# Kernel optimization log

Hardware: AMD Instinct MI355X
Metric: run time of the kernel (lower is better)

The kernel has to match this reference:

```python
import jax, jax.numpy as jnp
import numpy as np

N_MIX = 2


def setup_inputs() -> dict:
    key = jax.random.key(0)
    k1, k2, k3, k4 = jax.random.split(key, 4)
    B, d_k, N = 8, 512, 2048
    qt = jax.random.normal(k1, (B, d_k, N), dtype=jnp.float32)
    kt = jax.random.normal(k2, (B, d_k, N), dtype=jnp.float32)
    vt = jax.random.normal(k3, (B, d_k, N), dtype=jnp.float32)
    std = N_MIX ** -0.5
    weight = jax.random.uniform(k4, (N_MIX, d_k), dtype=jnp.float32, minval=-std, maxval=std)
    return {"qt": qt, "kt": kt, "vt": vt, "weight": weight}


def reference(qt, kt, vt, weight):
    # qt: [B, d_k, N], kt: [B, d_k, N2], vt: [B, d_v, N2], weight: [m, d_k]
    B, d_k, N = qt.shape
    N2 = kt.shape[2]
    m = N_MIX
    d = d_k // m
    temperature = jnp.float32(d_k ** 0.5)  # note: sqrt(d_k), not sqrt(d)

    # mixture weights pi: softmax over the m mixture components
    bar_qt = jnp.mean(qt, axis=2)  # [B, d_k]
    pi = jax.nn.softmax(jnp.einsum('md,bd->bm', weight, bar_qt), axis=1)  # [B, m]
    pi = pi.reshape(B * m, 1, 1)

    q = jnp.transpose(qt.reshape(B * m, d, N), (0, 2, 1))  # [B*m, N, d]
    k = kt.reshape(B * m, d, N2)                            # [B*m, d, N2]
    v = jnp.transpose(vt, (0, 2, 1))                        # [B, N2, d_v]

    attn = jnp.matmul(q, k) / temperature                   # [B*m, N, N2]
    attn = jax.nn.softmax(attn, axis=2)
    # dropout is identity at inference
    attn = (attn * pi).reshape(B, m, N, N2).sum(axis=1)     # [B, N, N2]

    output = jnp.matmul(attn, v)                            # [B, N, d_v]
    return output, attn
```

## Files before the change

kernel.cpp:

```cpp
#include <hip/hip_runtime.h>
#include <stdint.h>

typedef unsigned short u16;
typedef float f32x4 __attribute__((ext_vector_type(4)));
typedef _Float16 half8 __attribute__((ext_vector_type(8)));
typedef __fp16 fp16x2 __attribute__((ext_vector_type(2)));

#define B_  8
#define M_  2
#define DK_ 512
#define D_  256
#define N_  2048
#define DV_ 512

#define OUT_FLOATS (B_*N_*DV_)
#define QB_U16     (B_*M_*N_*D_)

__device__ __forceinline__ uint32_t pk16(float a, float b){
    fp16x2 h = __builtin_amdgcn_cvt_pkrtz(a, b);
    return __builtin_bit_cast(uint32_t, h);
}
__device__ __forceinline__ float h2f_lo(uint32_t u){
    return (float)__builtin_bit_cast(_Float16, (unsigned short)(u & 0xffffu));
}
__device__ __forceinline__ float h2f_hi(uint32_t u){
    return (float)__builtin_bit_cast(_Float16, (unsigned short)(u >> 16));
}

__global__ __launch_bounds__(256) void k0_transpose(const float* __restrict__ qt,
                                                    const float* __restrict__ kt,
                                                    u16* __restrict__ dstBase){
    const int it = blockIdx.x, yc = blockIdx.y, z = blockIdx.z;
    const int b = z & 7, src = z >> 3;
    const float* sp = src ? kt : qt;
    u16* dp = dstBase + (size_t)src * QB_U16;
    const int m = yc >> 2;
    const int cbase = (yc & 3) * 64;
    const int i0 = it * 64;
    __shared__ u16 lds[64 * 72];
    const int t = threadIdx.x;
    {
        const int c_loc = t >> 2;
        const int iq = (t & 3) * 16;
        const float* g = sp + (size_t)(b*DK_ + m*D_ + cbase + c_loc) * N_ + i0 + iq;
        float vv[16];
        *(float4*)&vv[0]  = *(const float4*)(g + 0);
        *(float4*)&vv[4]  = *(const float4*)(g + 4);
        *(float4*)&vv[8]  = *(const float4*)(g + 8);
        *(float4*)&vv[12] = *(const float4*)(g + 12);
        #pragma unroll
        for (int e = 0; e < 16; ++e){
            _Float16 hf = (_Float16)vv[e];
            lds[(iq + e)*72 + c_loc] = __builtin_bit_cast(unsigned short, hf);
        }
    }
    __syncthreads();
    {
        const int i_loc = t >> 2;
        const int cq = (t & 3) * 16;
        uint4 a  = *(const uint4*)&lds[i_loc*72 + cq];
        uint4 b2 = *(const uint4*)&lds[i_loc*72 + cq + 8];
        u16* o = dp + (size_t)((b*M_ + m)*N_ + i0 + i_loc) * D_ + cbase + cq;
        *(uint4*)o = a;
        *(uint4*)(o + 8) = b2;
    }
}

__global__ __launch_bounds__(256) void k0_vconv(const float* __restrict__ vt,
                                                u16* __restrict__ vB){
    size_t idx = ((size_t)blockIdx.x * 256 + threadIdx.x) * 8;
    const size_t total = (size_t)B_ * DV_ * N_;
    if (idx < total){
        float4 f0 = *(const float4*)(vt + idx);
        float4 f1 = *(const float4*)(vt + idx + 4);
        uint4 o;
        o.x = pk16(f0.x, f0.y);
        o.y = pk16(f0.z, f0.w);
        o.z = pk16(f1.x, f1.y);
        o.w = pk16(f1.z, f1.w);
        *(uint4*)(vB + idx) = o;
    }
}

__global__ __launch_bounds__(256) void k1_bar(const float* __restrict__ qt,
                                              float* __restrict__ bar){
    const int cg = blockIdx.x, b = blockIdx.y;
    const int t = threadIdx.x;
    const int c = cg*8 + (t >> 5);
    const int seg = t & 31;
    const float* g = qt + (size_t)(b*DK_ + c)*N_ + seg*64;
    float s = 0.f;
    #pragma unroll
    for (int k = 0; k < 16; ++k){
        float4 f = *(const float4*)(g + k*4);
        s += f.x + f.y + f.z + f.w;
    }
    s += __shfl_xor(s, 1); s += __shfl_xor(s, 2); s += __shfl_xor(s, 4);
    s += __shfl_xor(s, 8); s += __shfl_xor(s, 16);
    if (seg == 0) bar[b*DK_ + c] = s * (1.f / (float)N_);
}

__global__ void k2_logits(const float* __restrict__ wgt,
                          const float* __restrict__ bar,
                          float* __restrict__ wsLog){
    const int bm = blockIdx.x;
    const int b = bm >> 1, m = bm & 1;
    const int l = threadIdx.x;
    float s = 0.f;
    #pragma unroll
    for (int k = 0; k < 8; ++k){
        const int c = l + k*64;
        s += wgt[m*DK_ + c] * bar[b*DK_ + c];
    }
    s += __shfl_xor(s, 1); s += __shfl_xor(s, 2); s += __shfl_xor(s, 4);
    s += __shfl_xor(s, 8); s += __shfl_xor(s, 16); s += __shfl_xor(s, 32);
    if (l == 0) wsLog[bm] = s;
}

__global__ __launch_bounds__(256, 2) void k3_qk(const u16* __restrict__ qB,
                                                const u16* __restrict__ kB,
                                                uint32_t* __restrict__ attnE){
    const int jt = blockIdx.x, it = blockIdx.y, b = blockIdx.z;
    const int t = threadIdx.x;
    const int w = t >> 6, l = t & 63;
    const int wi = w & 1, wj = w >> 1;
    const int l15 = l & 15, lq = l >> 4;
    __shared__ u16 lds[4 * 128 * 64];

    f32x4 acc[2][4][4] = {};

    const int srow = t >> 1, shalf = t & 1;
    for (int bk = 0; bk < 4; ++bk){
        #pragma unroll
        for (int tile = 0; tile < 4; ++tile){
            const int qk = tile >> 1, m = tile & 1;
            const u16* sp = qk ? kB : qB;
            const int row0 = (qk ? jt : it) * 128;
            const u16* g = sp + (size_t)((b*M_ + m)*N_ + row0 + srow) * D_ + bk*64 + shalf*32;
            const uint4* gp = (const uint4*)g;
            uint4 v0 = gp[0], v1 = gp[1], v2 = gp[2], v3 = gp[3];
            u16* base = &lds[(tile*128 + srow) * 64];
            const int rs = srow & 7;
            *(uint4*)&base[((shalf*4 + 0) ^ rs) * 8] = v0;
            *(uint4*)&base[((shalf*4 + 1) ^ rs) * 8] = v1;
            *(uint4*)&base[((shalf*4 + 2) ^ rs) * 8] = v2;
            *(uint4*)&base[((shalf*4 + 3) ^ rs) * 8] = v3;
        }
        __syncthreads();
        #pragma unroll
        for (int ks = 0; ks < 2; ++ks){
            #pragma unroll
            for (int m = 0; m < 2; ++m){
                half8 a[4], bb[4];
                #pragma unroll
                for (int ti = 0; ti < 4; ++ti){
                    const int row = wi*64 + ti*16 + l15;
                    const int gr = (ks*4 + lq) ^ (row & 7);
                    a[ti] = *(const half8*)&lds[(m*128 + row)*64 + gr*8];
                }
                #pragma unroll
                for (int tj = 0; tj < 4; ++tj){
                    const int row = wj*64 + tj*16 + l15;
                    const int gr = (ks*4 + lq) ^ (row & 7);
                    bb[tj] = *(const half8*)&lds[((2 + m)*128 + row)*64 + gr*8];
                }
                #pragma unroll
                for (int ti = 0; ti < 4; ++ti)
                    #pragma unroll
                    for (int tj = 0; tj < 4; ++tj)
                        acc[m][ti][tj] = __builtin_amdgcn_mfma_f32_16x16x32_f16(
                            a[ti], bb[tj], acc[m][ti][tj], 0, 0, 0);
            }
        }
        __syncthreads();
    }

    const float INVT = 0.04419417382415922f;
    uint32_t* op = attnE + (size_t)b * N_ * N_;
    const int ibase = it*128 + wi*64;
    const int jbase = jt*128 + wj*64;
    #pragma unroll
    for (int ti = 0; ti < 4; ++ti){
        #pragma unroll
        for (int tj = 0; tj < 4; ++tj){
            #pragma unroll
            for (int rr = 0; rr < 4; ++rr){
                const int i = ibase + ti*16 + lq*4 + rr;
                const int j = jbase + tj*16 + l15;
                const float e0 = __expf(acc[0][ti][tj][rr] * INVT);
                const float e1 = __expf(acc[1][ti][tj][rr] * INVT);
                op[(size_t)i * N_ + j] = pk16(e0, e1);
            }
        }
    }
}

__global__ __launch_bounds__(256, 2) void k4_pv(const float* __restrict__ vt,
                                                const u16* __restrict__ vB,
                                                const float* __restrict__ wsLog,
                                                uint32_t* __restrict__ attnE,
                                                float* __restrict__ outO){
    const int itile = blockIdx.x, b = blockIdx.y;
    const int i0 = itile * 64;
    const int t = threadIdx.x, w = t >> 6, l = t & 63;
    const int l15 = l & 15, lq = l >> 4;
    __shared__ u16 v_lds[DV_ * 32];
    __shared__ float p0s[64], p1s[64];

    const float lg0 = wsLog[b*2 + 0], lg1 = wsLog[b*2 + 1];
    const float pi0 = 1.f / (1.f + __expf(lg1 - lg0));
    const float pi1 = 1.f / (1.f + __expf(lg0 - lg1));

    {
        const int rl = t >> 2, seg = t & 3;
        const uint4* e = (const uint4*)(attnE + (size_t)(b*N_ + i0 + rl)*N_ + seg*512);
        float s0 = 0.f, s1 = 0.f;
        for (int k = 0; k < 128; ++k){
            uint4 u = e[k];
            s0 += h2f_lo(u.x) + h2f_lo(u.y) + h2f_lo(u.z) + h2f_lo(u.w);
            s1 += h2f_hi(u.x) + h2f_hi(u.y) + h2f_hi(u.z) + h2f_hi(u.w);
        }
        s0 += __shfl_xor(s0, 1); s0 += __shfl_xor(s0, 2);
        s1 += __shfl_xor(s1, 1); s1 += __shfl_xor(s1, 2);
        if (seg == 0){ p0s[rl] = pi0 / s0; p1s[rl] = pi1 / s1; }
    }
    __syncthreads();

    f32x4 acc[32] = {};
    const int rl = w*16 + l15;
    const float p0 = p0s[rl], p1 = p1s[rl];
    uint32_t* erow = attnE + (size_t)(b*N_ + i0 + rl)*N_;

    for (int c = 0; c < 64; ++c){
        const int j0 = c * 32;
        {
            const int dv = t * 2;
            if (vB){
                const u16* g = vB + (size_t)(b*DV_ + dv)*N_ + j0;
                #pragma unroll
                for (int r = 0; r < 2; ++r){
                    const int dvr = dv + r;
                    const uint4* gp = (const uint4*)(g + (size_t)r * N_);
                    #pragma unroll
                    for (int q8 = 0; q8 < 4; ++q8)
                        *(uint4*)&v_lds[dvr*32 + ((q8 ^ (dvr & 3)) * 8)] = gp[q8];
                }
            } else {
                #pragma unroll
                for (int r = 0; r < 2; ++r){
                    const int dvr = dv + r;
                    const float* gr = vt + (size_t)(b*DV_ + dvr)*N_ + j0;
                    #pragma unroll
                    for (int q8 = 0; q8 < 4; ++q8){
                        float4 fA = *(const float4*)(gr + q8*8);
                        float4 fB = *(const float4*)(gr + q8*8 + 4);
                        uint4 u;
                        u.x = pk16(fA.x, fA.y);
                        u.y = pk16(fA.z, fA.w);
                        u.z = pk16(fB.x, fB.y);
                        u.w = pk16(fB.z, fB.w);
                        *(uint4*)&v_lds[dvr*32 + ((q8 ^ (dvr & 3)) * 8)] = u;
                    }
                }
            }
        }
        uint32_t* ep = erow + j0 + lq*8;
        uint4 u0 = *(const uint4*)ep;
        uint4 u1 = *(const uint4*)(ep + 4);
        float av[8];
        av[0] = p0*h2f_lo(u0.x) + p1*h2f_hi(u0.x);
        av[1] = p0*h2f_lo(u0.y) + p1*h2f_hi(u0.y);
        av[2] = p0*h2f_lo(u0.z) + p1*h2f_hi(u0.z);
        av[3] = p0*h2f_lo(u0.w) + p1*h2f_hi(u0.w);
        av[4] = p0*h2f_lo(u1.x) + p1*h2f_hi(u1.x);
        av[5] = p0*h2f_lo(u1.y) + p1*h2f_hi(u1.y);
        av[6] = p0*h2f_lo(u1.z) + p1*h2f_hi(u1.z);
        av[7] = p0*h2f_lo(u1.w) + p1*h2f_hi(u1.w);
        uint4 ua;
        ua.x = pk16(av[0], av[1]);
        ua.y = pk16(av[2], av[3]);
        ua.z = pk16(av[4], av[5]);
        ua.w = pk16(av[6], av[7]);
        union { uint4 u; half8 h; } cvt;
        cvt.u = ua;
        half8 af = cvt.h;

        __syncthreads();

        float4 w0 = make_float4(av[0], av[1], av[2], av[3]);
        float4 w1 = make_float4(av[4], av[5], av[6], av[7]);
        *(float4*)ep = w0;
        *(float4*)(ep + 4) = w1;

        #pragma unroll
        for (int n = 0; n < 32; ++n){
            const int dv = n*16 + l15;
            half8 bv = *(const half8*)&v_lds[dv*32 + ((lq ^ (dv & 3)) * 8)];
            acc[n] = __builtin_amdgcn_mfma_f32_16x16x32_f16(af, bv, acc[n], 0, 0, 0);
        }
        __syncthreads();
    }

    #pragma unroll
    for (int n = 0; n < 32; ++n){
        #pragma unroll
        for (int rr = 0; rr < 4; ++rr){
            const int i = i0 + w*16 + lq*4 + rr;
            const int dv = n*16 + l15;
            outO[(size_t)(b*N_ + i)*DV_ + dv] = acc[n][rr];
        }
    }
}

extern "C" void kernel_launch(void* const* d_in, const int* in_sizes, int n_in,
                              void* d_out, int out_size, void* d_ws, size_t ws_size,
                              hipStream_t stream){
    const float* qt  = (const float*)d_in[0];
    const float* kt  = (const float*)d_in[1];
    const float* vt  = (const float*)d_in[2];
    const float* wgt = (const float*)d_in[3];

    float* ws    = (float*)d_ws;
    float* wsLog = ws;
    float* wsBar = ws + 16;

    u16* stage = (u16*)d_out;
    u16* kB = stage + QB_U16;
    uint32_t* attnE = (uint32_t*)d_out + OUT_FLOATS;
    float* outO = (float*)d_out;

    const size_t vbBytes = (size_t)B_ * DV_ * N_ * 2;
    u16* vB = (ws_size >= (size_t)65536 + vbBytes)
                  ? (u16*)((char*)d_ws + 65536) : (u16*)nullptr;

    k0_transpose<<<dim3(32, 8, 16), 256, 0, stream>>>(qt, kt, stage);
    if (vB) k0_vconv<<<dim3(4096), 256, 0, stream>>>(vt, vB);
    k1_bar<<<dim3(64, 8), 256, 0, stream>>>(qt, wsBar);
    k2_logits<<<dim3(16), 64, 0, stream>>>(wgt, wsBar, wsLog);
    k3_qk<<<dim3(16, 16, 8), 256, 0, stream>>>(stage, kB, attnE);
    k4_pv<<<dim3(32, 8), 256, 0, stream>>>(vt, vB, wsLog, attnE, outO);
}
```

Baseline: 270.2 us.

## Split row-sum into separate kernel and double-buffer V tiles in PV kernel

Moves the per-row softmax denominator computation out of the PV kernel into a dedicated, fully parallel rowsum kernel that writes per-row scale factors to workspace. The PV kernel now runs 512 threads per block, with each half of the waves covering half the value dimension. It double-buffers V tiles in LDS, prefetching global loads two chunks ahead, and prefetches the next attention fragments. This removes the serial row-sum prologue and one barrier per iteration, at the cost of an extra launch, a second full read of the attention matrix, and doubled LDS use.

```diff
diff --git a/kernel.cpp b/kernel.cpp
--- a/kernel.cpp
+++ b/kernel.cpp
@@ -195,87 +195,124 @@
     }
 }
 
-__global__ __launch_bounds__(256, 2) void k4_pv(const float* __restrict__ vt,
-                                                const u16* __restrict__ vB,
-                                                const float* __restrict__ wsLog,
-                                                uint32_t* __restrict__ attnE,
-                                                float* __restrict__ outO){
+__global__ __launch_bounds__(256) void k35_rowsum(const uint32_t* __restrict__ attnE,
+                                                  const float* __restrict__ wsLog,
+                                                  float* __restrict__ wsScale){
+    const int blk = blockIdx.x;
+    const int b = blk >> 9;
+    const int w = threadIdx.x >> 6, l = threadIdx.x & 63;
+    const int i = (blk & 511)*4 + w;
+    const uint4* e = (const uint4*)(attnE + ((size_t)b*N_ + i)*N_);
+    float s0 = 0.f, s1 = 0.f;
+    #pragma unroll
+    for (int k = 0; k < 8; ++k){
+        uint4 u = e[k*64 + l];
+        s0 += h2f_lo(u.x) + h2f_lo(u.y) + h2f_lo(u.z) + h2f_lo(u.w);
+        s1 += h2f_hi(u.x) + h2f_hi(u.y) + h2f_hi(u.z) + h2f_hi(u.w);
+    }
+    s0 += __shfl_xor(s0, 1);  s1 += __shfl_xor(s1, 1);
+    s0 += __shfl_xor(s0, 2);  s1 += __shfl_xor(s1, 2);
+    s0 += __shfl_xor(s0, 4);  s1 += __shfl_xor(s1, 4);
+    s0 += __shfl_xor(s0, 8);  s1 += __shfl_xor(s1, 8);
+    s0 += __shfl_xor(s0, 16); s1 += __shfl_xor(s1, 16);
+    s0 += __shfl_xor(s0, 32); s1 += __shfl_xor(s1, 32);
+    if (l == 0){
+        const float lg0 = wsLog[b*2 + 0], lg1 = wsLog[b*2 + 1];
+        const float pi0 = 1.f / (1.f + __expf(lg1 - lg0));
+        const float pi1 = 1.f / (1.f + __expf(lg0 - lg1));
+        wsScale[((size_t)b*N_ + i)*2 + 0] = pi0 / s0;
+        wsScale[((size_t)b*N_ + i)*2 + 1] = pi1 / s1;
+    }
+}
+
+template<bool HASVB>
+__global__ __launch_bounds__(512) void k4_pv(const float* __restrict__ vt,
+                                             const u16* __restrict__ vB,
+                                             const float* __restrict__ wsScale,
+                                             uint32_t* __restrict__ attnE,
+                                             float* __restrict__ outO){
     const int itile = blockIdx.x, b = blockIdx.y;
     const int i0 = itile * 64;
-    const int t = threadIdx.x, w = t >> 6, l = t & 63;
+    const int t = threadIdx.x;
+    const int l = t & 63, w = t >> 6;
     const int l15 = l & 15, lq = l >> 4;
-    __shared__ u16 v_lds[DV_ * 32];
-    __shared__ float p0s[64], p1s[64];
-
-    const float lg0 = wsLog[b*2 + 0], lg1 = wsLog[b*2 + 1];
-    const float pi0 = 1.f / (1.f + __expf(lg1 - lg0));
-    const float pi1 = 1.f / (1.f + __expf(lg0 - lg1));
-
-    {
-        const int rl = t >> 2, seg = t & 3;
-        const uint4* e = (const uint4*)(attnE + (size_t)(b*N_ + i0 + rl)*N_ + seg*512);
-        float s0 = 0.f, s1 = 0.f;
-        for (int k = 0; k < 128; ++k){
-            uint4 u = e[k];
-            s0 += h2f_lo(u.x) + h2f_lo(u.y) + h2f_lo(u.z) + h2f_lo(u.w);
-            s1 += h2f_hi(u.x) + h2f_hi(u.y) + h2f_hi(u.z) + h2f_hi(u.w);
-        }
-        s0 += __shfl_xor(s0, 1); s0 += __shfl_xor(s0, 2);
-        s1 += __shfl_xor(s1, 1); s1 += __shfl_xor(s1, 2);
-        if (seg == 0){ p0s[rl] = pi0 / s0; p1s[rl] = pi1 / s1; }
-    }
+    const int rowgrp = w & 3, dvh = w >> 2;
+    __shared__ u16 v_lds[2][512 * 32];
+
+    const int rl = rowgrp*16 + l15;
+    const float2 p01 = *(const float2*)&wsScale[((size_t)(b*N_ + i0 + rl))*2];
+    const float p0 = p01.x, p1 = p01.y;
+    uint32_t* erow = attnE + (size_t)(b*N_ + i0 + rl) * N_;
+
+    const int vswz  = (t >> 2) & 3;
+    const int rslot = lq ^ (l15 >> 2);
+
+    const u16*   gv16 = vB + (size_t)(b*DV_ + t)*N_;
+    const float* gv32 = vt + (size_t)(b*DV_ + t)*N_;
+
+    uint4  rv[4];
+    float4 rf[8];
+
+    auto issue_load = [&](int c){
+        const int j0 = c*32;
+        if (HASVB){
+            const uint4* gp = (const uint4*)(gv16 + j0);
+            rv[0] = gp[0]; rv[1] = gp[1]; rv[2] = gp[2]; rv[3] = gp[3];
+        } else {
+            const float4* gp = (const float4*)(gv32 + j0);
+            #pragma unroll
+            for (int q = 0; q < 8; ++q) rf[q] = gp[q];
+        }
+    };
+    auto write_lds = [&](int buf){
+        u16* base = &v_lds[buf][t*32];
+        #pragma unroll
+        for (int G = 0; G < 4; ++G){
+            uint4 u;
+            if (HASVB){
+                u = rv[G];
+            } else {
+                u.x = pk16(rf[2*G].x,   rf[2*G].y);
+                u.y = pk16(rf[2*G].z,   rf[2*G].w);
+                u.z = pk16(rf[2*G+1].x, rf[2*G+1].y);
+                u.w = pk16(rf[2*G+1].z, rf[2*G+1].w);
+            }
+            *(uint4*)&base[(G ^ vswz)*8] = u;
+        }
+    };
+
+    f32x4 acc[16] = {};
+
+    issue_load(0);
+    write_lds(0);
+    issue_load(1);
+    uint4 e0 = *(const uint4*)(erow + lq*8);
+    uint4 e1 = *(const uint4*)(erow + lq*8 + 4);
     __syncthreads();
 
-    f32x4 acc[32] = {};
-    const int rl = w*16 + l15;
-    const float p0 = p0s[rl], p1 = p1s[rl];
-    uint32_t* erow = attnE + (size_t)(b*N_ + i0 + rl)*N_;
-
+    int cur = 0;
     for (int c = 0; c < 64; ++c){
-        const int j0 = c * 32;
-        {
-            const int dv = t * 2;
-            if (vB){
-                const u16* g = vB + (size_t)(b*DV_ + dv)*N_ + j0;
-                #pragma unroll
-                for (int r = 0; r < 2; ++r){
-                    const int dvr = dv + r;
-                    const uint4* gp = (const uint4*)(g + (size_t)r * N_);
-                    #pragma unroll
-                    for (int q8 = 0; q8 < 4; ++q8)
-                        *(uint4*)&v_lds[dvr*32 + ((q8 ^ (dvr & 3)) * 8)] = gp[q8];
-                }
-            } else {
-                #pragma unroll
-                for (int r = 0; r < 2; ++r){
-                    const int dvr = dv + r;
-                    const float* gr = vt + (size_t)(b*DV_ + dvr)*N_ + j0;
-                    #pragma unroll
-                    for (int q8 = 0; q8 < 4; ++q8){
-                        float4 fA = *(const float4*)(gr + q8*8);
-                        float4 fB = *(const float4*)(gr + q8*8 + 4);
-                        uint4 u;
-                        u.x = pk16(fA.x, fA.y);
-                        u.y = pk16(fA.z, fA.w);
-                        u.z = pk16(fB.x, fB.y);
-                        u.w = pk16(fB.z, fB.w);
-                        *(uint4*)&v_lds[dvr*32 + ((q8 ^ (dvr & 3)) * 8)] = u;
-                    }
-                }
-            }
-        }
-        uint32_t* ep = erow + j0 + lq*8;
-        uint4 u0 = *(const uint4*)ep;
-        uint4 u1 = *(const uint4*)(ep + 4);
+        if (c + 1 < 64) write_lds(cur ^ 1);
+        if (c + 2 < 64) issue_load(c + 2);
+        uint4 en0, en1;
+        if (c + 1 < 64){
+            en0 = *(const uint4*)(erow + (c+1)*32 + lq*8);
+            en1 = *(const uint4*)(erow + (c+1)*32 + lq*8 + 4);
+        }
         float av[8];
-        av[0] = p0*h2f_lo(u0.x) + p1*h2f_hi(u0.x);
-        av[1] = p0*h2f_lo(u0.y) + p1*h2f_hi(u0.y);
-        av[2] = p0*h2f_lo(u0.z) + p1*h2f_hi(u0.z);
-        av[3] = p0*h2f_lo(u0.w) + p1*h2f_hi(u0.w);
-        av[4] = p0*h2f_lo(u1.x) + p1*h2f_hi(u1.x);
-        av[5] = p0*h2f_lo(u1.y) + p1*h2f_hi(u1.y);
-        av[6] = p0*h2f_lo(u1.z) + p1*h2f_hi(u1.z);
-        av[7] = p0*h2f_lo(u1.w) + p1*h2f_hi(u1.w);
+        av[0] = p0*h2f_lo(e0.x) + p1*h2f_hi(e0.x);
+        av[1] = p0*h2f_lo(e0.y) + p1*h2f_hi(e0.y);
+        av[2] = p0*h2f_lo(e0.z) + p1*h2f_hi(e0.z);
+        av[3] = p0*h2f_lo(e0.w) + p1*h2f_hi(e0.w);
+        av[4] = p0*h2f_lo(e1.x) + p1*h2f_hi(e1.x);
+        av[5] = p0*h2f_lo(e1.y) + p1*h2f_hi(e1.y);
+        av[6] = p0*h2f_lo(e1.z) + p1*h2f_hi(e1.z);
+        av[7] = p0*h2f_lo(e1.w) + p1*h2f_hi(e1.w);
+        if (dvh == 0){
+            float* ap = (float*)(erow + c*32 + lq*8);
+            *(float4*)ap       = make_float4(av[0], av[1], av[2], av[3]);
+            *(float4*)(ap + 4) = make_float4(av[4], av[5], av[6], av[7]);
+        }
         uint4 ua;
         ua.x = pk16(av[0], av[1]);
         ua.y = pk16(av[2], av[3]);
@@ -285,28 +322,23 @@
         cvt.u = ua;
         half8 af = cvt.h;
 
+        const u16* vb = &v_lds[cur][(dvh*256 + l15)*32 + rslot*8];
+        #pragma unroll
+        for (int n = 0; n < 16; ++n){
+            half8 bv = *(const half8*)(vb + n*512);
+            acc[n] = __builtin_amdgcn_mfma_f32_16x16x32_f16(af, bv, acc[n], 0, 0, 0);
+        }
+        if (c + 1 < 64){ e0 = en0; e1 = en1; }
         __syncthreads();
-
-        float4 w0 = make_float4(av[0], av[1], av[2], av[3]);
-        float4 w1 = make_float4(av[4], av[5], av[6], av[7]);
-        *(float4*)ep = w0;
-        *(float4*)(ep + 4) = w1;
-
-        #pragma unroll
-        for (int n = 0; n < 32; ++n){
-            const int dv = n*16 + l15;
-            half8 bv = *(const half8*)&v_lds[dv*32 + ((lq ^ (dv & 3)) * 8)];
-            acc[n] = __builtin_amdgcn_mfma_f32_16x16x32_f16(af, bv, acc[n], 0, 0, 0);
-        }
-        __syncthreads();
-    }
-
-    #pragma unroll
-    for (int n = 0; n < 32; ++n){
+        cur ^= 1;
+    }
+
+    #pragma unroll
+    for (int n = 0; n < 16; ++n){
         #pragma unroll
         for (int rr = 0; rr < 4; ++rr){
-            const int i = i0 + w*16 + lq*4 + rr;
-            const int dv = n*16 + l15;
+            const int i  = i0 + rowgrp*16 + lq*4 + rr;
+            const int dv = dvh*256 + n*16 + l15;
             outO[(size_t)(b*N_ + i)*DV_ + dv] = acc[n][rr];
         }
     }
@@ -320,9 +352,10 @@
     const float* vt  = (const float*)d_in[2];
     const float* wgt = (const float*)d_in[3];
 
-    float* ws    = (float*)d_ws;
-    float* wsLog = ws;
-    float* wsBar = ws + 16;
+    float* ws      = (float*)d_ws;
+    float* wsLog   = ws;
+    float* wsBar   = ws + 16;
+    float* wsScale = (float*)((char*)d_ws + 32768);
 
     u16* stage = (u16*)d_out;
     u16* kB = stage + QB_U16;
@@ -330,13 +363,15 @@
     float* outO = (float*)d_out;
 
     const size_t vbBytes = (size_t)B_ * DV_ * N_ * 2;
-    u16* vB = (ws_size >= (size_t)65536 + vbBytes)
-                  ? (u16*)((char*)d_ws + 65536) : (u16*)nullptr;
+    u16* vB = (ws_size >= (size_t)262144 + vbBytes)
+                  ? (u16*)((char*)d_ws + 262144) : (u16*)nullptr;
 
     k0_transpose<<<dim3(32, 8, 16), 256, 0, stream>>>(qt, kt, stage);
     if (vB) k0_vconv<<<dim3(4096), 256, 0, stream>>>(vt, vB);
     k1_bar<<<dim3(64, 8), 256, 0, stream>>>(qt, wsBar);
     k2_logits<<<dim3(16), 64, 0, stream>>>(wgt, wsBar, wsLog);
     k3_qk<<<dim3(16, 16, 8), 256, 0, stream>>>(stage, kB, attnE);
-    k4_pv<<<dim3(32, 8), 256, 0, stream>>>(vt, vB, wsLog, attnE, outO);
-}
+    k35_rowsum<<<dim3(4096), 256, 0, stream>>>(attnE, wsLog, wsScale);
+    if (vB) k4_pv<true ><<<dim3(32, 8), 512, 0, stream>>>(vt, vB, wsScale, attnE, outO);
+    else    k4_pv<false><<<dim3(32, 8), 512, 0, stream>>>(vt, vB, wsScale, attnE, outO);
+}
```

Measured after the change: 238.4 us. 1.13x faster.

## Fuse row-sum and mean into producers; register-pipeline PV kernel without LDS

Applied to the files above, without the earlier changes.

The query column mean moves into the transpose kernel via atomics, dropping the separate mean kernel. Softmax row sums are now accumulated with atomics in the QK epilogue, so the PV kernel no longer re-reads each attention row just to normalise it. The PV kernel is restructured into 32-row tiles with the value dimension split across waves, loading V fragments straight from global into registers with double buffering instead of staging through LDS. In exchange it adds a workspace memset, atomic contention and more register pressure, and each wave reloads V from global memory.

```diff
diff --git a/kernel.cpp b/kernel.cpp
--- a/kernel.cpp
+++ b/kernel.cpp
@@ -29,7 +29,8 @@
 
 __global__ __launch_bounds__(256) void k0_transpose(const float* __restrict__ qt,
                                                     const float* __restrict__ kt,
-                                                    u16* __restrict__ dstBase){
+                                                    u16* __restrict__ dstBase,
+                                                    float* __restrict__ wsBar){
     const int it = blockIdx.x, yc = blockIdx.y, z = blockIdx.z;
     const int b = z & 7, src = z >> 3;
     const float* sp = src ? kt : qt;
@@ -53,6 +54,15 @@
             _Float16 hf = (_Float16)vv[e];
             lds[(iq + e)*72 + c_loc] = __builtin_bit_cast(unsigned short, hf);
         }
+        if (src == 0){
+            float s = 0.f;
+            #pragma unroll
+            for (int e = 0; e < 16; ++e) s += vv[e];
+            s += __shfl_xor(s, 1);
+            s += __shfl_xor(s, 2);
+            if ((t & 3) == 0)
+                atomicAdd(&wsBar[b*DK_ + m*D_ + cbase + c_loc], s);
+        }
     }
     __syncthreads();
     {
@@ -82,24 +92,6 @@
     }
 }
 
-__global__ __launch_bounds__(256) void k1_bar(const float* __restrict__ qt,
-                                              float* __restrict__ bar){
-    const int cg = blockIdx.x, b = blockIdx.y;
-    const int t = threadIdx.x;
-    const int c = cg*8 + (t >> 5);
-    const int seg = t & 31;
-    const float* g = qt + (size_t)(b*DK_ + c)*N_ + seg*64;
-    float s = 0.f;
-    #pragma unroll
-    for (int k = 0; k < 16; ++k){
-        float4 f = *(const float4*)(g + k*4);
-        s += f.x + f.y + f.z + f.w;
-    }
-    s += __shfl_xor(s, 1); s += __shfl_xor(s, 2); s += __shfl_xor(s, 4);
-    s += __shfl_xor(s, 8); s += __shfl_xor(s, 16);
-    if (seg == 0) bar[b*DK_ + c] = s * (1.f / (float)N_);
-}
-
 __global__ void k2_logits(const float* __restrict__ wgt,
                           const float* __restrict__ bar,
                           float* __restrict__ wsLog){
@@ -114,12 +106,13 @@
     }
     s += __shfl_xor(s, 1); s += __shfl_xor(s, 2); s += __shfl_xor(s, 4);
     s += __shfl_xor(s, 8); s += __shfl_xor(s, 16); s += __shfl_xor(s, 32);
-    if (l == 0) wsLog[bm] = s;
+    if (l == 0) wsLog[bm] = s * (1.f / (float)N_);
 }
 
 __global__ __launch_bounds__(256, 2) void k3_qk(const u16* __restrict__ qB,
                                                 const u16* __restrict__ kB,
-                                                uint32_t* __restrict__ attnE){
+                                                uint32_t* __restrict__ attnE,
+                                                float* __restrict__ wsSum){
     const int jt = blockIdx.x, it = blockIdx.y, b = blockIdx.z;
     const int t = threadIdx.x;
     const int w = t >> 6, l = t & 63;
@@ -181,6 +174,7 @@
     const int jbase = jt*128 + wj*64;
     #pragma unroll
     for (int ti = 0; ti < 4; ++ti){
+        float rs[2][4] = {};
         #pragma unroll
         for (int tj = 0; tj < 4; ++tj){
             #pragma unroll
@@ -190,124 +184,144 @@
                 const float e0 = __expf(acc[0][ti][tj][rr] * INVT);
                 const float e1 = __expf(acc[1][ti][tj][rr] * INVT);
                 op[(size_t)i * N_ + j] = pk16(e0, e1);
-            }
-        }
-    }
-}
-
+                rs[0][rr] += e0;
+                rs[1][rr] += e1;
+            }
+        }
+        #pragma unroll
+        for (int m2 = 0; m2 < 2; ++m2){
+            #pragma unroll
+            for (int rr = 0; rr < 4; ++rr){
+                float s = rs[m2][rr];
+                s += __shfl_xor(s, 1); s += __shfl_xor(s, 2);
+                s += __shfl_xor(s, 4); s += __shfl_xor(s, 8);
+                if (l15 == 0)
+                    atomicAdd(&wsSum[(size_t)(b*M_ + m2)*N_ + ibase + ti*16 + lq*4 + rr], s);
+            }
+        }
+    }
+}
+
+template<bool HASVB>
 __global__ __launch_bounds__(256, 2) void k4_pv(const float* __restrict__ vt,
                                                 const u16* __restrict__ vB,
                                                 const float* __restrict__ wsLog,
+                                                const float* __restrict__ wsSum,
                                                 uint32_t* __restrict__ attnE,
                                                 float* __restrict__ outO){
-    const int itile = blockIdx.x, b = blockIdx.y;
-    const int i0 = itile * 64;
-    const int t = threadIdx.x, w = t >> 6, l = t & 63;
+    const int tile = blockIdx.x, b = blockIdx.y;
+    const int i0 = tile * 32;
+    const int t = threadIdx.x, l = t & 63;
+    const int dvq = t >> 6;
     const int l15 = l & 15, lq = l >> 4;
-    __shared__ u16 v_lds[DV_ * 32];
-    __shared__ float p0s[64], p1s[64];
 
     const float lg0 = wsLog[b*2 + 0], lg1 = wsLog[b*2 + 1];
     const float pi0 = 1.f / (1.f + __expf(lg1 - lg0));
     const float pi1 = 1.f / (1.f + __expf(lg0 - lg1));
 
-    {
-        const int rl = t >> 2, seg = t & 3;
-        const uint4* e = (const uint4*)(attnE + (size_t)(b*N_ + i0 + rl)*N_ + seg*512);
-        float s0 = 0.f, s1 = 0.f;
-        for (int k = 0; k < 128; ++k){
-            uint4 u = e[k];
-            s0 += h2f_lo(u.x) + h2f_lo(u.y) + h2f_lo(u.z) + h2f_lo(u.w);
-            s1 += h2f_hi(u.x) + h2f_hi(u.y) + h2f_hi(u.z) + h2f_hi(u.w);
-        }
-        s0 += __shfl_xor(s0, 1); s0 += __shfl_xor(s0, 2);
-        s1 += __shfl_xor(s1, 1); s1 += __shfl_xor(s1, 2);
-        if (seg == 0){ p0s[rl] = pi0 / s0; p1s[rl] = pi1 / s1; }
-    }
-    __syncthreads();
-
-    f32x4 acc[32] = {};
-    const int rl = w*16 + l15;
-    const float p0 = p0s[rl], p1 = p1s[rl];
-    uint32_t* erow = attnE + (size_t)(b*N_ + i0 + rl)*N_;
-
-    for (int c = 0; c < 64; ++c){
-        const int j0 = c * 32;
-        {
-            const int dv = t * 2;
-            if (vB){
-                const u16* g = vB + (size_t)(b*DV_ + dv)*N_ + j0;
-                #pragma unroll
-                for (int r = 0; r < 2; ++r){
-                    const int dvr = dv + r;
-                    const uint4* gp = (const uint4*)(g + (size_t)r * N_);
-                    #pragma unroll
-                    for (int q8 = 0; q8 < 4; ++q8)
-                        *(uint4*)&v_lds[dvr*32 + ((q8 ^ (dvr & 3)) * 8)] = gp[q8];
-                }
+    float p0[2], p1[2];
+    uint32_t* erow[2];
+    #pragma unroll
+    for (int rg = 0; rg < 2; ++rg){
+        const int row = i0 + rg*16 + l15;
+        p0[rg] = pi0 / wsSum[(size_t)(b*M_ + 0)*N_ + row];
+        p1[rg] = pi1 / wsSum[(size_t)(b*M_ + 1)*N_ + row];
+        erow[rg] = attnE + (size_t)(b*N_ + row) * N_;
+    }
+
+    const u16*   vb16 = vB + (size_t)(b*DV_ + dvq*128 + l15)*N_ + lq*8;
+    const float* vb32 = vt + (size_t)(b*DV_ + dvq*128 + l15)*N_ + lq*8;
+
+    f32x4 acc[2][8] = {};
+    uint4 eA[2][2], eB[2][2];
+    half8 bA[8], bB[8];
+
+    auto loadE = [&](uint4 (&e)[2][2], int c){
+        #pragma unroll
+        for (int rg = 0; rg < 2; ++rg){
+            const uint4* p = (const uint4*)(erow[rg] + c*32 + lq*8);
+            e[rg][0] = p[0];
+            e[rg][1] = p[1];
+        }
+    };
+    auto loadB = [&](half8 (&bb)[8], int c){
+        #pragma unroll
+        for (int n = 0; n < 8; ++n){
+            if (HASVB){
+                bb[n] = *(const half8*)(vb16 + (size_t)n*16*N_ + c*32);
             } else {
-                #pragma unroll
-                for (int r = 0; r < 2; ++r){
-                    const int dvr = dv + r;
-                    const float* gr = vt + (size_t)(b*DV_ + dvr)*N_ + j0;
-                    #pragma unroll
-                    for (int q8 = 0; q8 < 4; ++q8){
-                        float4 fA = *(const float4*)(gr + q8*8);
-                        float4 fB = *(const float4*)(gr + q8*8 + 4);
-                        uint4 u;
-                        u.x = pk16(fA.x, fA.y);
-                        u.y = pk16(fA.z, fA.w);
-                        u.z = pk16(fB.x, fB.y);
-                        u.w = pk16(fB.z, fB.w);
-                        *(uint4*)&v_lds[dvr*32 + ((q8 ^ (dvr & 3)) * 8)] = u;
-                    }
-                }
-            }
-        }
-        uint32_t* ep = erow + j0 + lq*8;
-        uint4 u0 = *(const uint4*)ep;
-        uint4 u1 = *(const uint4*)(ep + 4);
-        float av[8];
-        av[0] = p0*h2f_lo(u0.x) + p1*h2f_hi(u0.x);
-        av[1] = p0*h2f_lo(u0.y) + p1*h2f_hi(u0.y);
-        av[2] = p0*h2f_lo(u0.z) + p1*h2f_hi(u0.z);
-        av[3] = p0*h2f_lo(u0.w) + p1*h2f_hi(u0.w);
-        av[4] = p0*h2f_lo(u1.x) + p1*h2f_hi(u1.x);
-        av[5] = p0*h2f_lo(u1.y) + p1*h2f_hi(u1.y);
-        av[6] = p0*h2f_lo(u1.z) + p1*h2f_hi(u1.z);
-        av[7] = p0*h2f_lo(u1.w) + p1*h2f_hi(u1.w);
-        uint4 ua;
-        ua.x = pk16(av[0], av[1]);
-        ua.y = pk16(av[2], av[3]);
-        ua.z = pk16(av[4], av[5]);
-        ua.w = pk16(av[6], av[7]);
-        union { uint4 u; half8 h; } cvt;
-        cvt.u = ua;
-        half8 af = cvt.h;
-
-        __syncthreads();
-
-        float4 w0 = make_float4(av[0], av[1], av[2], av[3]);
-        float4 w1 = make_float4(av[4], av[5], av[6], av[7]);
-        *(float4*)ep = w0;
-        *(float4*)(ep + 4) = w1;
-
-        #pragma unroll
-        for (int n = 0; n < 32; ++n){
-            const int dv = n*16 + l15;
-            half8 bv = *(const half8*)&v_lds[dv*32 + ((lq ^ (dv & 3)) * 8)];
-            acc[n] = __builtin_amdgcn_mfma_f32_16x16x32_f16(af, bv, acc[n], 0, 0, 0);
-        }
-        __syncthreads();
+                const float* p = vb32 + (size_t)n*16*N_ + c*32;
+                float4 f0 = *(const float4*)p;
+                float4 f1 = *(const float4*)(p + 4);
+                uint4 u;
+                u.x = pk16(f0.x, f0.y); u.y = pk16(f0.z, f0.w);
+                u.z = pk16(f1.x, f1.y); u.w = pk16(f1.z, f1.w);
+                union { uint4 u; half8 h; } cv; cv.u = u;
+                bb[n] = cv.h;
+            }
+        }
+    };
+
+    loadE(eA, 0);
+    loadB(bA, 0);
+
+    auto body = [&](int c, uint4 (&ec)[2][2], uint4 (&en)[2][2],
+                    half8 (&bc)[8], half8 (&bn)[8]){
+        float av[2][8];
+        half8 af[2];
+        #pragma unroll
+        for (int rg = 0; rg < 2; ++rg){
+            uint4 u0 = ec[rg][0], u1 = ec[rg][1];
+            av[rg][0] = p0[rg]*h2f_lo(u0.x) + p1[rg]*h2f_hi(u0.x);
+            av[rg][1] = p0[rg]*h2f_lo(u0.y) + p1[rg]*h2f_hi(u0.y);
+            av[rg][2] = p0[rg]*h2f_lo(u0.z) + p1[rg]*h2f_hi(u0.z);
+            av[rg][3] = p0[rg]*h2f_lo(u0.w) + p1[rg]*h2f_hi(u0.w);
+            av[rg][4] = p0[rg]*h2f_lo(u1.x) + p1[rg]*h2f_hi(u1.x);
+            av[rg][5] = p0[rg]*h2f_lo(u1.y) + p1[rg]*h2f_hi(u1.y);
+            av[rg][6] = p0[rg]*h2f_lo(u1.z) + p1[rg]*h2f_hi(u1.z);
+            av[rg][7] = p0[rg]*h2f_lo(u1.w) + p1[rg]*h2f_hi(u1.w);
+            uint4 ua;
+            ua.x = pk16(av[rg][0], av[rg][1]);
+            ua.y = pk16(av[rg][2], av[rg][3]);
+            ua.z = pk16(av[rg][4], av[rg][5]);
+            ua.w = pk16(av[rg][6], av[rg][7]);
+            union { uint4 u; half8 h; } cv; cv.u = ua;
+            af[rg] = cv.h;
+        }
+        __builtin_amdgcn_sched_barrier(0);
+        __builtin_amdgcn_s_barrier();
+        __builtin_amdgcn_sched_barrier(0);
+        if (dvq < 2){
+            float* ap = (float*)(erow[dvq] + c*32 + lq*8);
+            *(float4*)ap       = make_float4(av[dvq][0], av[dvq][1], av[dvq][2], av[dvq][3]);
+            *(float4*)(ap + 4) = make_float4(av[dvq][4], av[dvq][5], av[dvq][6], av[dvq][7]);
+        }
+        if (c < 63){
+            loadE(en, c + 1);
+            loadB(bn, c + 1);
+        }
+        #pragma unroll
+        for (int n = 0; n < 8; ++n){
+            acc[0][n] = __builtin_amdgcn_mfma_f32_16x16x32_f16(af[0], bc[n], acc[0][n], 0, 0, 0);
+            acc[1][n] = __builtin_amdgcn_mfma_f32_16x16x32_f16(af[1], bc[n], acc[1][n], 0, 0, 0);
+        }
+    };
+
+    for (int c = 0; c < 64; c += 2){
+        body(c,     eA, eB, bA, bB);
+        body(c + 1, eB, eA, bB, bA);
     }
 
     #pragma unroll
-    for (int n = 0; n < 32; ++n){
-        #pragma unroll
-        for (int rr = 0; rr < 4; ++rr){
-            const int i = i0 + w*16 + lq*4 + rr;
-            const int dv = n*16 + l15;
-            outO[(size_t)(b*N_ + i)*DV_ + dv] = acc[n][rr];
+    for (int n = 0; n < 8; ++n){
+        #pragma unroll
+        for (int rg = 0; rg < 2; ++rg){
+            #pragma unroll
+            for (int rr = 0; rr < 4; ++rr){
+                const int i  = i0 + rg*16 + lq*4 + rr;
+                const int dv = dvq*128 + n*16 + l15;
+                outO[(size_t)(b*N_ + i)*DV_ + dv] = acc[rg][n][rr];
+            }
         }
     }
 }
@@ -322,7 +336,8 @@
 
     float* ws    = (float*)d_ws;
     float* wsLog = ws;
-    float* wsBar = ws + 16;
+    float* wsBar = (float*)((char*)d_ws + 4096);
+    float* wsSum = (float*)((char*)d_ws + 65536);
 
     u16* stage = (u16*)d_out;
     u16* kB = stage + QB_U16;
@@ -330,13 +345,15 @@
     float* outO = (float*)d_out;
 
     const size_t vbBytes = (size_t)B_ * DV_ * N_ * 2;
-    u16* vB = (ws_size >= (size_t)65536 + vbBytes)
-                  ? (u16*)((char*)d_ws + 65536) : (u16*)nullptr;
-
-    k0_transpose<<<dim3(32, 8, 16), 256, 0, stream>>>(qt, kt, stage);
+    u16* vB = (ws_size >= (size_t)1048576 + vbBytes)
+                  ? (u16*)((char*)d_ws + 1048576) : (u16*)nullptr;
+
+    hipMemsetAsync(d_ws, 0, 262144, stream);
+
+    k0_transpose<<<dim3(32, 8, 16), 256, 0, stream>>>(qt, kt, stage, wsBar);
     if (vB) k0_vconv<<<dim3(4096), 256, 0, stream>>>(vt, vB);
-    k1_bar<<<dim3(64, 8), 256, 0, stream>>>(qt, wsBar);
     k2_logits<<<dim3(16), 64, 0, stream>>>(wgt, wsBar, wsLog);
-    k3_qk<<<dim3(16, 16, 8), 256, 0, stream>>>(stage, kB, attnE);
-    k4_pv<<<dim3(32, 8), 256, 0, stream>>>(vt, vB, wsLog, attnE, outO);
-}
+    k3_qk<<<dim3(16, 16, 8), 256, 0, stream>>>(stage, kB, attnE, wsSum);
+    if (vB) k4_pv<true ><<<dim3(64, 8), 256, 0, stream>>>(vt, vB, wsLog, wsSum, attnE, outO);
+    else    k4_pv<false><<<dim3(64, 8), 256, 0, stream>>>(vt, vB, wsLog, wsSum, attnE, outO);
+}
```

New measurement: 304.5 us. 12.7% more time.
